# Kernel tuning notes

Measured on AMD Instinct MI355X. Metric: run time of the kernel, lower is better.

The kernel has to match this reference:

```python
import jax, jax.numpy as jnp
import numpy as np
from jax import lax

# Shared Conv2d [1,1] + BN + ReLU is represented as a per-point affine (BN folded
# into conv weight/bias at eval) followed by ReLU, matching inference-mode math.

B, N1, N2, K = 8, 8192, 2048, 8
C1, C2 = 64, 128
MLP0, MLP1, MLP2 = 128, 128, 128  # mlp=[128,128], mlp2=[128]


def setup_inputs() -> dict:
    key = jax.random.key(0)
    ks = jax.random.split(key, 10)
    sc = lambda fan_in: 1.0 / np.sqrt(fan_in)
    return {
        "xyz1": jax.random.normal(ks[0], (B, N1, 3), jnp.float32),
        "xyz2": jax.random.normal(ks[1], (B, N2, 3), jnp.float32),
        "feat1": jax.random.normal(ks[2], (B, N1, C1), jnp.float32),
        "feat2": jax.random.normal(ks[3], (B, N2, C2), jnp.float32),
        "W0": jax.random.normal(ks[4], (C2 + 3, MLP0), jnp.float32) * sc(C2 + 3),
        "b0": jnp.zeros((MLP0,), jnp.float32),
        "W1": jax.random.normal(ks[5], (MLP0, MLP1), jnp.float32) * sc(MLP0),
        "b1": jnp.zeros((MLP1,), jnp.float32),
        "W2": jax.random.normal(ks[6], (MLP1 + C1, MLP2), jnp.float32) * sc(MLP1 + C1),
        "b2": jnp.zeros((MLP2,), jnp.float32),
    }


def _knn_idx(xyz1, xyz2, k):
    # squared distances (B, N1, N2); top-k nearest in xyz2 for each xyz1 point
    d2 = jnp.sum((xyz1[:, :, None, :] - xyz2[:, None, :, :]) ** 2, axis=-1)
    _, idx = lax.top_k(-d2, k)  # (B, N1, K)
    return idx


def _gather(src, idx):
    # src: (B, N2, C), idx: (B, N1, K) -> (B, N1, K, C)
    return jax.vmap(lambda s, i: s[i])(src, idx)


def reference(xyz1, xyz2, feat1, feat2, W0, b0, W1, b1, W2, b2):
    idx = _knn_idx(xyz1, xyz2, K)
    xyz2_g = _gather(xyz2, idx)            # (B, N1, K, 3)
    feat2_g = _gather(feat2, idx)          # (B, N1, K, C2)
    xyz_diff = xyz2_g - xyz1[:, :, None, :]
    net = jnp.concatenate([feat2_g, xyz_diff], axis=-1)  # (B, N1, K, C2+3)
    net = jax.nn.relu(net @ W0 + b0)
    net = jax.nn.relu(net @ W1 + b1)       # (B, N1, K, MLP1)
    pooled = jnp.max(net, axis=2)          # max pooling over neighbors
    cat = jnp.concatenate([pooled, feat1], axis=-1)      # (B, N1, MLP1+C1)
    out = jax.nn.relu(cat @ W2 + b2)       # (B, N1, MLP2)
    return out
```

## Files before the change

### kernel.cpp

```cpp
#include <hip/hip_runtime.h>
#include <hip/hip_bf16.h>

constexpr int B_  = 8;
constexpr int N1_ = 8192;
constexpr int N2_ = 2048;
constexpr int K_  = 8;

typedef short bf16x8 __attribute__((ext_vector_type(8)));
typedef float f32x4  __attribute__((ext_vector_type(4)));

__device__ __forceinline__ short f2b(float x) {
    __hip_bfloat16 h = __float2bfloat16(x);
    return *reinterpret_cast<short*>(&h);
}

#define CASU(a, b) { const unsigned _lo = (a) < (b) ? (a) : (b); \
                     const unsigned _hi = (a) < (b) ? (b) : (a); \
                     (a) = _lo; (b) = _hi; }

__global__ __launch_bounds__(256) void prep_feat2(const float* __restrict__ feat2,
                                                  short* __restrict__ feat2b) {
    const int i = blockIdx.x * 256 + threadIdx.x;
    const float4 v = ((const float4*)feat2)[i];
    uint2 o;
    o.x = (unsigned short)f2b(v.x) | ((unsigned)(unsigned short)f2b(v.y) << 16);
    o.y = (unsigned short)f2b(v.z) | ((unsigned)(unsigned short)f2b(v.w) << 16);
    ((uint2*)feat2b)[i] = o;
}

__global__ __launch_bounds__(256) void prep_weights(
    const float* __restrict__ W0, const float* __restrict__ W1,
    const float* __restrict__ W2, const float* __restrict__ xyz2,
    short* __restrict__ W0T, short* __restrict__ W1T, short* __restrict__ W2T,
    float4* __restrict__ xpack) {
    int i = blockIdx.x * 256 + threadIdx.x;
    if (i < 128 * 160) {
        const int n = i / 160, k = i % 160;
        W0T[i] = (k < 131) ? f2b(W0[k * 128 + n]) : (short)0;
        return;
    }
    i -= 128 * 160;
    if (i < 128 * 128) {
        const int n = i >> 7, k = i & 127;
        W1T[i] = f2b(W1[k * 128 + n]);
        return;
    }
    i -= 128 * 128;
    if (i < 128 * 192) {
        const int n = i / 192, k = i % 192;
        W2T[i] = f2b(W2[k * 128 + n]);
        return;
    }
    i -= 128 * 192;
    xpack[i] = make_float4(xyz2[i * 3 + 0], xyz2[i * 3 + 1], xyz2[i * 3 + 2], 0.f);
}

constexpr int LCAP = 76;

__global__ __launch_bounds__(256) void knn_lazy(const float* __restrict__ xyz1,
                                                const float4* __restrict__ xpack,
                                                int* __restrict__ idx) {
    __shared__ __align__(16) unsigned short sMem[78 * 256];
    float* sD = (float*)sMem;
    int*   sI = (int*)sMem + 64 * 33;

    const int b = blockIdx.y;
    const int lane = threadIdx.x & 63;
    const int s = threadIdx.x >> 6;
    const int tid = threadIdx.x;
    const int n = blockIdx.x * 64 + lane;

    const float* q = xyz1 + ((size_t)b * N1_ + n) * 3;
    const float qx = q[0], qy = q[1], qz = q[2];
    const float4* P = xpack + (size_t)b * N2_ + s * 512;

    unsigned bd[K_];
#pragma unroll
    for (int t = 0; t < K_; ++t) bd[t] = __float_as_uint(3.0e38f);
    int cnt = 0;

    for (int j0 = 0; j0 < 512; j0 += 8) {
        unsigned xu[8];
#pragma unroll
        for (int u = 0; u < 8; ++u) {
#pragma clang fp contract(off)
            const float4 p = P[j0 + u];
            const float dx = qx - p.x;
            const float dy = qy - p.y;
            const float dz = qz - p.z;
            const float dx2 = dx * dx;
            const float dy2 = dy * dy;
            const float dz2 = dz * dz;
            xu[u] = __float_as_uint((dx2 + dy2) + dz2);
        }
        const unsigned thr = bd[K_ - 1];
#pragma unroll
        for (int u = 0; u < 8; ++u) {
            const bool acc = xu[u] < thr;
            const int capped = cnt < LCAP ? cnt : LCAP;
            const int slot = acc ? capped : (LCAP + 1);
            sMem[slot * 256 + tid] = (unsigned short)(j0 + u);
            cnt += acc ? 1 : 0;
        }
        CASU(xu[0], xu[1]); CASU(xu[2], xu[3]); CASU(xu[4], xu[5]); CASU(xu[6], xu[7]);
        CASU(xu[0], xu[2]); CASU(xu[1], xu[3]); CASU(xu[4], xu[6]); CASU(xu[5], xu[7]);
        CASU(xu[1], xu[2]); CASU(xu[5], xu[6]); CASU(xu[0], xu[4]); CASU(xu[3], xu[7]);
        CASU(xu[1], xu[5]); CASU(xu[2], xu[6]);
        CASU(xu[1], xu[4]); CASU(xu[3], xu[6]);
        CASU(xu[2], xu[4]); CASU(xu[3], xu[5]);
        CASU(xu[3], xu[4]);
        unsigned t0 = bd[0] < xu[7] ? bd[0] : xu[7];
        unsigned t1 = bd[1] < xu[6] ? bd[1] : xu[6];
        unsigned t2 = bd[2] < xu[5] ? bd[2] : xu[5];
        unsigned t3 = bd[3] < xu[4] ? bd[3] : xu[4];
        unsigned t4 = bd[4] < xu[3] ? bd[4] : xu[3];
        unsigned t5 = bd[5] < xu[2] ? bd[5] : xu[2];
        unsigned t6 = bd[6] < xu[1] ? bd[6] : xu[1];
        unsigned t7 = bd[7] < xu[0] ? bd[7] : xu[0];
        CASU(t0, t4); CASU(t1, t5); CASU(t2, t6); CASU(t3, t7);
        CASU(t0, t2); CASU(t1, t3); CASU(t4, t6); CASU(t5, t7);
        CASU(t0, t1); CASU(t2, t3); CASU(t4, t5); CASU(t6, t7);
        bd[0] = t0; bd[1] = t1; bd[2] = t2; bd[3] = t3;
        bd[4] = t4; bd[5] = t5; bd[6] = t6; bd[7] = t7;
    }

    float rd[K_];
    int   ri[K_];
#pragma unroll
    for (int t = 0; t < K_; ++t) { rd[t] = 3.0e38f; ri[t] = 0; }
    const int m = cnt < LCAP ? cnt : LCAP;
    for (int t = 0;; ++t) {
        const bool act = t < m;
        if (!__any(act)) break;
        if (act) {
#pragma clang fp contract(off)
            const int jl = sMem[t * 256 + tid];
            const float4 p = P[jl];
            const float dx = qx - p.x;
            const float dy = qy - p.y;
            const float dz = qz - p.z;
            const float dx2 = dx * dx;
            const float dy2 = dy * dy;
            const float dz2 = dz * dz;
            const float d2 = (dx2 + dy2) + dz2;
            if (d2 < rd[K_ - 1]) {
                rd[K_ - 1] = d2; ri[K_ - 1] = s * 512 + jl;
#pragma unroll
                for (int t2 = K_ - 1; t2 >= 1; --t2) {
                    if (rd[t2] < rd[t2 - 1]) {
                        float td = rd[t2]; rd[t2] = rd[t2 - 1]; rd[t2 - 1] = td;
                        int   ti = ri[t2]; ri[t2] = ri[t2 - 1]; ri[t2 - 1] = ti;
                    }
                }
            }
        }
    }

    if (__any(cnt > LCAP)) {
        if (cnt > LCAP) {
#pragma unroll
            for (int t = 0; t < K_; ++t) { rd[t] = 3.0e38f; ri[t] = 0; }
            for (int j = 0; j < 512; ++j) {
#pragma clang fp contract(off)
                const float4 p = P[j];
                const float dx = qx - p.x;
                const float dy = qy - p.y;
                const float dz = qz - p.z;
                const float dx2 = dx * dx;
                const float dy2 = dy * dy;
                const float dz2 = dz * dz;
                const float d2 = (dx2 + dy2) + dz2;
                if (d2 < rd[K_ - 1]) {
                    rd[K_ - 1] = d2; ri[K_ - 1] = s * 512 + j;
#pragma unroll
                    for (int t2 = K_ - 1; t2 >= 1; --t2) {
                        if (rd[t2] < rd[t2 - 1]) {
                            float td = rd[t2]; rd[t2] = rd[t2 - 1]; rd[t2 - 1] = td;
                            int   ti = ri[t2]; ri[t2] = ri[t2 - 1]; ri[t2 - 1] = ti;
                        }
                    }
                }
            }
        }
    }

    __syncthreads();
#pragma unroll
    for (int t = 0; t < K_; ++t) {
        sD[lane * 33 + s * 8 + t] = rd[t];
        sI[lane * 33 + s * 8 + t] = ri[t];
    }
    __syncthreads();

    if (tid < 64) {
        const int qq = tid;
        int h[4] = {0, 0, 0, 0};
        const int base = (b * N1_ + n) * K_;
#pragma unroll
        for (int t = 0; t < K_; ++t) {
            float best = 3.1e38f;
            int   bidx = 0, bs = 0;
#pragma unroll
            for (int ss = 0; ss < 4; ++ss) {
                if (h[ss] < 8) {
                    const float d = sD[qq * 33 + ss * 8 + h[ss]];
                    if (d < best) { best = d; bidx = sI[qq * 33 + ss * 8 + h[ss]]; bs = ss; }
                }
            }
            h[bs]++;
            idx[base + t] = bidx;
        }
    }
}

__global__ __launch_bounds__(256) void fused_mfma(
    const float* __restrict__ xyz1, const float* __restrict__ xyz2,
    const float* __restrict__ feat1,
    const float* __restrict__ b0, const float* __restrict__ b1,
    const float* __restrict__ b2,
    const short* __restrict__ feat2b, const short* __restrict__ W0T,
    const short* __restrict__ W1T, const short* __restrict__ W2T,
    const int* __restrict__ idx, float* __restrict__ out) {
    __shared__ __align__(16) short sA[128 * 168];
    __shared__ __align__(16) short sCat[16 * 200];

    const int b = blockIdx.y;
    const int n0 = blockIdx.x * 16;
    const int tid = threadIdx.x;

    {
        const int row = tid >> 1, half = tid & 1;
        const int p = row >> 3, kk = row & 7;
        const int n = n0 + p;
        const int j = idx[((size_t)b * N1_ + n) * K_ + kk];
        const uint4* src = (const uint4*)(feat2b + ((size_t)(b * N2_ + j)) * 128 + half * 64);
        uint4* dst = (uint4*)(sA + row * 168 + half * 64);
#pragma unroll
        for (int t = 0; t < 8; ++t) dst[t] = src[t];
        uint4* pad = (uint4*)(sA + row * 168 + 128 + half * 16);
        if (half == 0) {
            const float dx = xyz2[((size_t)b * N2_ + j) * 3 + 0] - xyz1[((size_t)b * N1_ + n) * 3 + 0];
            const float dy = xyz2[((size_t)b * N2_ + j) * 3 + 1] - xyz1[((size_t)b * N1_ + n) * 3 + 1];
            const float dz = xyz2[((size_t)b * N2_ + j) * 3 + 2] - xyz1[((size_t)b * N1_ + n) * 3 + 2];
            uint4 v;
            v.x = (unsigned short)f2b(dx) | ((unsigned)(unsigned short)f2b(dy) << 16);
            v.y = (unsigned short)f2b(dz);
            v.z = 0; v.w = 0;
            pad[0] = v;
            pad[1] = make_uint4(0, 0, 0, 0);
        } else {
            pad[0] = make_uint4(0, 0, 0, 0);
            pad[1] = make_uint4(0, 0, 0, 0);
        }
    }
    {
#pragma unroll
        for (int u = 0; u < 4; ++u) {
            const int e = tid * 4 + u;
            const int p = e >> 6, c = e & 63;
            sCat[p * 200 + 128 + c] = f2b(feat1[((size_t)b * N1_ + n0 + p) * 64 + c]);
        }
    }
    __syncthreads();

    const int wave = tid >> 6, lane = tid & 63;
    const int q = lane >> 4, l15 = lane & 15;
    const int mBase = (wave & 1) * 64, nBase = (wave >> 1) * 64;

    const f32x4 zero4 = {0.f, 0.f, 0.f, 0.f};

    f32x4 acc[4][4];
#pragma unroll
    for (int mt = 0; mt < 4; ++mt)
#pragma unroll
        for (int nt = 0; nt < 4; ++nt) acc[mt][nt] = zero4;

    for (int ks = 0; ks < 5; ++ks) {
        bf16x8 af[4], bf[4];
#pragma unroll
        for (int mt = 0; mt < 4; ++mt)
            af[mt] = *(const bf16x8*)(sA + (mBase + mt * 16 + l15) * 168 + ks * 32 + q * 8);
#pragma unroll
        for (int nt = 0; nt < 4; ++nt)
            bf[nt] = *(const bf16x8*)(W0T + (nBase + nt * 16 + l15) * 160 + ks * 32 + q * 8);
#pragma unroll
        for (int mt = 0; mt < 4; ++mt)
#pragma unroll
            for (int nt = 0; nt < 4; ++nt)
                acc[mt][nt] = __builtin_amdgcn_mfma_f32_16x16x32_bf16(af[mt], bf[nt], acc[mt][nt], 0, 0, 0);
    }

    float b0v[4];
#pragma unroll
    for (int nt = 0; nt < 4; ++nt) b0v[nt] = b0[nBase + nt * 16 + l15];
    __syncthreads();
#pragma unroll
    for (int mt = 0; mt < 4; ++mt)
#pragma unroll
        for (int nt = 0; nt < 4; ++nt)
#pragma unroll
            for (int r = 0; r < 4; ++r) {
                const int row = mBase + mt * 16 + q * 4 + r;
                const int col = nBase + nt * 16 + l15;
                sA[row * 136 + col] = f2b(fmaxf(acc[mt][nt][r] + b0v[nt], 0.0f));
            }
    __syncthreads();

    f32x4 acc2[4][4];
#pragma unroll
    for (int mt = 0; mt < 4; ++mt)
#pragma unroll
        for (int nt = 0; nt < 4; ++nt) acc2[mt][nt] = zero4;

    for (int ks = 0; ks < 4; ++ks) {
        bf16x8 af[4], bf[4];
#pragma unroll
        for (int mt = 0; mt < 4; ++mt)
            af[mt] = *(const bf16x8*)(sA + (mBase + mt * 16 + l15) * 136 + ks * 32 + q * 8);
#pragma unroll
        for (int nt = 0; nt < 4; ++nt)
            bf[nt] = *(const bf16x8*)(W1T + (nBase + nt * 16 + l15) * 128 + ks * 32 + q * 8);
#pragma unroll
        for (int mt = 0; mt < 4; ++mt)
#pragma unroll
            for (int nt = 0; nt < 4; ++nt)
                acc2[mt][nt] = __builtin_amdgcn_mfma_f32_16x16x32_bf16(af[mt], bf[nt], acc2[mt][nt], 0, 0, 0);
    }

    float b1v[4];
#pragma unroll
    for (int nt = 0; nt < 4; ++nt) b1v[nt] = b1[nBase + nt * 16 + l15];
#pragma unroll
    for (int mt = 0; mt < 4; ++mt)
#pragma unroll
        for (int nt = 0; nt < 4; ++nt) {
            float vm = fmaxf(acc2[mt][nt][0] + b1v[nt], 0.0f);
#pragma unroll
            for (int r = 1; r < 4; ++r) vm = fmaxf(vm, acc2[mt][nt][r] + b1v[nt]);
            const float other = __shfl_xor(vm, 16);
            const float pool = fmaxf(vm, other);
            if ((q & 1) == 0) {
                const int pp = (mBase >> 3) + mt * 2 + (q >> 1);
                sCat[pp * 200 + nBase + nt * 16 + l15] = f2b(pool);
            }
        }
    __syncthreads();

    f32x4 acc3[2];
    acc3[0] = zero4; acc3[1] = zero4;
    const int nB2 = wave * 32;
    for (int ks = 0; ks < 6; ++ks) {
        const bf16x8 a2 = *(const bf16x8*)(sCat + l15 * 200 + ks * 32 + q * 8);
#pragma unroll
        for (int nt = 0; nt < 2; ++nt) {
            const bf16x8 b2f = *(const bf16x8*)(W2T + (nB2 + nt * 16 + l15) * 192 + ks * 32 + q * 8);
            acc3[nt] = __builtin_amdgcn_mfma_f32_16x16x32_bf16(a2, b2f, acc3[nt], 0, 0, 0);
        }
    }
    float b2v[2];
#pragma unroll
    for (int nt = 0; nt < 2; ++nt) b2v[nt] = b2[nB2 + nt * 16 + l15];
#pragma unroll
    for (int nt = 0; nt < 2; ++nt)
#pragma unroll
        for (int r = 0; r < 4; ++r) {
            const int p = q * 4 + r;
            const int col = nB2 + nt * 16 + l15;
            out[((size_t)(b * N1_ + n0 + p)) * 128 + col] = fmaxf(acc3[nt][r] + b2v[nt], 0.0f);
        }
}

extern "C" void kernel_launch(void* const* d_in, const int* in_sizes, int n_in,
                              void* d_out, int out_size, void* d_ws, size_t ws_size,
                              hipStream_t stream) {
    const float* xyz1  = (const float*)d_in[0];
    const float* xyz2  = (const float*)d_in[1];
    const float* feat1 = (const float*)d_in[2];
    const float* feat2 = (const float*)d_in[3];
    const float* W0    = (const float*)d_in[4];
    const float* b0    = (const float*)d_in[5];
    const float* W1    = (const float*)d_in[6];
    const float* b1    = (const float*)d_in[7];
    const float* W2    = (const float*)d_in[8];
    const float* b2    = (const float*)d_in[9];
    float* out = (float*)d_out;

    char* ws = (char*)d_ws;
    int*    idx    = (int*)(ws + 0);
    short*  feat2b = (short*)(ws + 2097152);
    short*  W0T    = (short*)(ws + 6291456);
    short*  W1T    = (short*)(ws + 6332416);
    short*  W2T    = (short*)(ws + 6365184);
    float4* xpack  = (float4*)(ws + 6414336);

    prep_feat2<<<2048, 256, 0, stream>>>(feat2, feat2b);
    prep_weights<<<304, 256, 0, stream>>>(W0, W1, W2, xyz2, W0T, W1T, W2T, xpack);
    knn_lazy<<<dim3(N1_ / 64, B_), 256, 0, stream>>>(xyz1, xpack, idx);
    fused_mfma<<<dim3(N1_ / 16, B_), 256, 0, stream>>>(xyz1, xyz2, feat1, b0, b1, b2,
                                                       feat2b, W0T, W1T, W2T, idx, out);
}
```

Baseline: 325.4 us.

## Split KNN scan into eight 256-point segments with byte candidate lists

The KNN kernel now splits the reference points into 8 segments of 256 per query instead of 4 of 512, with 32 queries per block. Each segment scan is shorter, candidate indices fit in bytes so the shared-memory buffer shrinks, and there are twice as many blocks. The first-pass distance now allows FMA contraction, with a small ULP slack on the threshold so the exact recheck still catches all true candidates. The final merge now combines 8 sorted lists instead of 4, which is more serial work for a few threads and adds some fallback risk if the smaller candidate cap overflows.

Result: slower. 368.6 us (+13.3%).

```diff
diff --git a/kernel.cpp b/kernel.cpp
--- a/kernel.cpp
+++ b/kernel.cpp
@@ -55,51 +55,49 @@
     xpack[i] = make_float4(xyz2[i * 3 + 0], xyz2[i * 3 + 1], xyz2[i * 3 + 2], 0.f);
 }
 
-constexpr int LCAP = 76;
+constexpr int SEG   = 256;
+constexpr int QPB   = 32;
+constexpr int LCAP2 = 56;
 
 __global__ __launch_bounds__(256) void knn_lazy(const float* __restrict__ xyz1,
                                                 const float4* __restrict__ xpack,
                                                 int* __restrict__ idx) {
-    __shared__ __align__(16) unsigned short sMem[78 * 256];
-    float* sD = (float*)sMem;
-    int*   sI = (int*)sMem + 64 * 33;
+    __shared__ __align__(16) unsigned char sBuf[16640];
+    float* sD = (float*)sBuf;
+    int*   sI = (int*)(sBuf + 8320);
 
     const int b = blockIdx.y;
-    const int lane = threadIdx.x & 63;
-    const int s = threadIdx.x >> 6;
+    const int ql  = threadIdx.x & 31;
+    const int s   = threadIdx.x >> 5;
     const int tid = threadIdx.x;
-    const int n = blockIdx.x * 64 + lane;
+    const int n = blockIdx.x * QPB + ql;
 
     const float* q = xyz1 + ((size_t)b * N1_ + n) * 3;
     const float qx = q[0], qy = q[1], qz = q[2];
-    const float4* P = xpack + (size_t)b * N2_ + s * 512;
+    const float4* P = xpack + (size_t)b * N2_ + s * SEG;
 
     unsigned bd[K_];
 #pragma unroll
     for (int t = 0; t < K_; ++t) bd[t] = __float_as_uint(3.0e38f);
     int cnt = 0;
 
-    for (int j0 = 0; j0 < 512; j0 += 8) {
+    for (int j0 = 0; j0 < SEG; j0 += 8) {
         unsigned xu[8];
 #pragma unroll
         for (int u = 0; u < 8; ++u) {
-#pragma clang fp contract(off)
             const float4 p = P[j0 + u];
             const float dx = qx - p.x;
             const float dy = qy - p.y;
             const float dz = qz - p.z;
-            const float dx2 = dx * dx;
-            const float dy2 = dy * dy;
-            const float dz2 = dz * dz;
-            xu[u] = __float_as_uint((dx2 + dy2) + dz2);
-        }
-        const unsigned thr = bd[K_ - 1];
+            xu[u] = __float_as_uint(dx * dx + dy * dy + dz * dz);
+        }
+        const unsigned thr = bd[K_ - 1] + 256u;
 #pragma unroll
         for (int u = 0; u < 8; ++u) {
             const bool acc = xu[u] < thr;
-            const int capped = cnt < LCAP ? cnt : LCAP;
-            const int slot = acc ? capped : (LCAP + 1);
-            sMem[slot * 256 + tid] = (unsigned short)(j0 + u);
+            const int capped = cnt < LCAP2 ? cnt : LCAP2;
+            const int slot = acc ? capped : (LCAP2 + 1);
+            sBuf[slot * 256 + tid] = (unsigned char)(j0 + u);
             cnt += acc ? 1 : 0;
         }
         CASU(xu[0], xu[1]); CASU(xu[2], xu[3]); CASU(xu[4], xu[5]); CASU(xu[6], xu[7]);
@@ -128,13 +126,13 @@
     int   ri[K_];
 #pragma unroll
     for (int t = 0; t < K_; ++t) { rd[t] = 3.0e38f; ri[t] = 0; }
-    const int m = cnt < LCAP ? cnt : LCAP;
+    const int m = cnt < LCAP2 ? cnt : LCAP2;
     for (int t = 0;; ++t) {
         const bool act = t < m;
         if (!__any(act)) break;
         if (act) {
 #pragma clang fp contract(off)
-            const int jl = sMem[t * 256 + tid];
+            const int jl = sBuf[t * 256 + tid];
             const float4 p = P[jl];
             const float dx = qx - p.x;
             const float dy = qy - p.y;
@@ -144,7 +142,7 @@
             const float dz2 = dz * dz;
             const float d2 = (dx2 + dy2) + dz2;
             if (d2 < rd[K_ - 1]) {
-                rd[K_ - 1] = d2; ri[K_ - 1] = s * 512 + jl;
+                rd[K_ - 1] = d2; ri[K_ - 1] = s * SEG + jl;
 #pragma unroll
                 for (int t2 = K_ - 1; t2 >= 1; --t2) {
                     if (rd[t2] < rd[t2 - 1]) {
@@ -156,11 +154,11 @@
         }
     }
 
-    if (__any(cnt > LCAP)) {
-        if (cnt > LCAP) {
+    if (__any(cnt > LCAP2)) {
+        if (cnt > LCAP2) {
 #pragma unroll
             for (int t = 0; t < K_; ++t) { rd[t] = 3.0e38f; ri[t] = 0; }
-            for (int j = 0; j < 512; ++j) {
+            for (int j = 0; j < SEG; ++j) {
 #pragma clang fp contract(off)
                 const float4 p = P[j];
                 const float dx = qx - p.x;
@@ -171,7 +169,7 @@
                 const float dz2 = dz * dz;
                 const float d2 = (dx2 + dy2) + dz2;
                 if (d2 < rd[K_ - 1]) {
-                    rd[K_ - 1] = d2; ri[K_ - 1] = s * 512 + j;
+                    rd[K_ - 1] = d2; ri[K_ - 1] = s * SEG + j;
 #pragma unroll
                     for (int t2 = K_ - 1; t2 >= 1; --t2) {
                         if (rd[t2] < rd[t2 - 1]) {
@@ -187,27 +185,29 @@
     __syncthreads();
 #pragma unroll
     for (int t = 0; t < K_; ++t) {
-        sD[lane * 33 + s * 8 + t] = rd[t];
-        sI[lane * 33 + s * 8 + t] = ri[t];
-    }
-    __syncthreads();
-
-    if (tid < 64) {
+        sD[ql * 65 + s * 8 + t] = rd[t];
+        sI[ql * 65 + s * 8 + t] = ri[t];
+    }
+    __syncthreads();
+
+    if (tid < QPB) {
         const int qq = tid;
-        int h[4] = {0, 0, 0, 0};
-        const int base = (b * N1_ + n) * K_;
+        const int nq = blockIdx.x * QPB + qq;
+        int h[8] = {0, 0, 0, 0, 0, 0, 0, 0};
+        const int base = (b * N1_ + nq) * K_;
 #pragma unroll
         for (int t = 0; t < K_; ++t) {
             float best = 3.1e38f;
             int   bidx = 0, bs = 0;
 #pragma unroll
-            for (int ss = 0; ss < 4; ++ss) {
+            for (int ss = 0; ss < 8; ++ss) {
                 if (h[ss] < 8) {
-                    const float d = sD[qq * 33 + ss * 8 + h[ss]];
-                    if (d < best) { best = d; bidx = sI[qq * 33 + ss * 8 + h[ss]]; bs = ss; }
+                    const float d = sD[qq * 65 + ss * 8 + h[ss]];
+                    if (d < best) { best = d; bidx = sI[qq * 65 + ss * 8 + h[ss]]; bs = ss; }
                 }
             }
-            h[bs]++;
+#pragma unroll
+            for (int ss = 0; ss < 8; ++ss) h[ss] += (ss == bs) ? 1 : 0;
             idx[base + t] = bidx;
         }
     }
@@ -395,7 +395,7 @@
 
     prep_feat2<<<2048, 256, 0, stream>>>(feat2, feat2b);
     prep_weights<<<304, 256, 0, stream>>>(W0, W1, W2, xyz2, W0T, W1T, W2T, xpack);
-    knn_lazy<<<dim3(N1_ / 64, B_), 256, 0, stream>>>(xyz1, xpack, idx);
+    knn_lazy<<<dim3(N1_ / QPB, B_), 256, 0, stream>>>(xyz1, xpack, idx);
     fused_mfma<<<dim3(N1_ / 16, B_), 256, 0, stream>>>(xyz1, xyz2, feat1, b0, b1, b2,
                                                        feat2b, W0T, W1T, W2T, idx, out);
 }
```
